# Kernel optimization log

Measured on AMD Instinct MI355X. Metric: run time of the kernel, lower is better.

## Reference

```python
import jax, jax.numpy as jnp
import numpy as np

N = 100000   # nodes
E = 1600000  # edges (avg degree 16)
IN, HID, OUT = 128, 128, 40


def setup_inputs() -> dict:
    key = jax.random.key(0)
    ks = jax.random.split(key, 7)
    return {
        "features": jax.random.normal(ks[0], (N, IN), jnp.float32),
        "src": jax.random.randint(ks[1], (E,), 0, N, jnp.int32),
        "dst": jax.random.randint(ks[2], (E,), 0, N, jnp.int32),
        "W1": jax.random.normal(ks[3], (IN, HID), jnp.float32) / np.sqrt(IN).astype(np.float32),
        "Wh": jax.random.normal(ks[4], (HID, HID), jnp.float32) / np.sqrt(HID).astype(np.float32),
        "W2": jax.random.normal(ks[5], (HID, OUT), jnp.float32) / np.sqrt(HID).astype(np.float32),
        "b2": jnp.zeros((OUT,), jnp.float32),
    }


def _agg(x, src, dst):
    # message passing: gather source node features along edges, sum-scatter to dst
    return jax.ops.segment_sum(x[src], dst, num_segments=N)


def reference(features, src, dst, W1, Wh, W2, b2):
    ones = jnp.ones((E,), jnp.float32)
    out_deg = jnp.clip(jax.ops.segment_sum(ones, src, num_segments=N), 1.0)
    in_deg = jnp.clip(jax.ops.segment_sum(ones, dst, num_segments=N), 1.0)
    lnorm = out_deg[:, None] ** -0.5  # 'both' left norm (src out-degree)
    rnorm = in_deg[:, None] ** -0.5   # 'both' right norm (dst in-degree)

    # conv1: GraphConv(norm='none', bias=False) -> plain sum aggregation, then relu
    h = jax.nn.relu(_agg(features @ W1, src, dst))
    # hidden GraphConv(norm='both', bias=False) + relu (dropout = identity in eval)
    h = jax.nn.relu(_agg((h * lnorm) @ Wh, src, dst) * rnorm)
    # conv2: GraphConv(norm='both', bias=True)
    h = _agg((h * lnorm) @ W2, src, dst) * rnorm + b2
    return jax.nn.log_softmax(h, axis=1)
```

## Files before the change

kernel.cpp:

```cpp
#include <hip/hip_runtime.h>
#include <math.h>

#define MAXDEG 64
#define BCAP 8192
#define EPB 4096

typedef __attribute__((ext_vector_type(8))) short bf16x8;
typedef __attribute__((ext_vector_type(4))) float f32x4;

static __device__ inline unsigned short f2bf(float f) {
    unsigned int u = __float_as_uint(f);
    u += 0x7FFFu + ((u >> 16) & 1u);
    return (unsigned short)(u >> 16);
}
static __device__ inline float bf2f(unsigned short u) {
    return __uint_as_float(((unsigned int)u) << 16);
}
static __device__ inline float4 ld_f4(const float* p) { return *(const float4*)p; }

static __device__ __forceinline__ void acc8(float* a, uint4 u) {
    a[0] += __uint_as_float(u.x << 16);
    a[1] += __uint_as_float(u.x & 0xFFFF0000u);
    a[2] += __uint_as_float(u.y << 16);
    a[3] += __uint_as_float(u.y & 0xFFFF0000u);
    a[4] += __uint_as_float(u.z << 16);
    a[5] += __uint_as_float(u.z & 0xFFFF0000u);
    a[6] += __uint_as_float(u.w << 16);
    a[7] += __uint_as_float(u.w & 0xFFFF0000u);
}

static __global__ __launch_bounds__(256) void wtrans_kernel(
    const float* __restrict__ W1, const float* __restrict__ Wh,
    const float* __restrict__ W2,
    unsigned short* __restrict__ W1t, unsigned short* __restrict__ WhT,
    unsigned short* __restrict__ Wt2) {
    int b = blockIdx.x;
    int t = threadIdx.x;
    if (b == 2) {
        for (int i = t; i < 48 * 128; i += 256) Wt2[i] = 0;
        __syncthreads();
        int n0 = (t & 31) * 4;
        if (n0 < 40) {
            for (int k = t >> 5; k < 128; k += 8) {
                float4 v = ld_f4(&W2[(size_t)k * 40 + n0]);
                Wt2[(size_t)(n0 + 0) * 128 + k] = f2bf(v.x);
                Wt2[(size_t)(n0 + 1) * 128 + k] = f2bf(v.y);
                Wt2[(size_t)(n0 + 2) * 128 + k] = f2bf(v.z);
                Wt2[(size_t)(n0 + 3) * 128 + k] = f2bf(v.w);
            }
        }
        return;
    }
    const float* Wsrc = (b == 0) ? W1 : Wh;
    unsigned short* Wdst = (b == 0) ? W1t : WhT;
    int n0 = (t & 31) * 4;
    for (int k = t >> 5; k < 128; k += 8) {
        float4 v = ld_f4(&Wsrc[(size_t)k * 128 + n0]);
        Wdst[(size_t)(n0 + 0) * 128 + k] = f2bf(v.x);
        Wdst[(size_t)(n0 + 1) * 128 + k] = f2bf(v.y);
        Wdst[(size_t)(n0 + 2) * 128 + k] = f2bf(v.z);
        Wdst[(size_t)(n0 + 3) * 128 + k] = f2bf(v.w);
    }
}

static __device__ __forceinline__ void gemm128_mfma256(
    const unsigned short* sa16, const unsigned short* __restrict__ Wt,
    unsigned short* __restrict__ Y, int row0, int t, int N) {
    int l = t & 63, w = t >> 6;
    int m = l & 15, kg = l >> 4;
    int row = w * 16 + m;
    int rsw = row & 15;
    f32x4 acc[8];
#pragma unroll
    for (int c = 0; c < 8; ++c) acc[c] = (f32x4){0.f, 0.f, 0.f, 0.f};
#pragma unroll
    for (int ks = 0; ks < 4; ++ks) {
        bf16x8 a = *(const bf16x8*)&sa16[(size_t)row * 128 + (((ks * 4 + kg) ^ rsw) * 8)];
        int kk = ks * 32 + kg * 8;
#pragma unroll
        for (int c = 0; c < 8; ++c) {
            bf16x8 b = *(const bf16x8*)&Wt[(size_t)(c * 16 + m) * 128 + kk];
            acc[c] = __builtin_amdgcn_mfma_f32_16x16x32_bf16(a, b, acc[c], 0, 0, 0);
        }
    }
#pragma unroll
    for (int c = 0; c < 8; ++c) {
        int col = c * 16 + m;
#pragma unroll
        for (int r = 0; r < 4; ++r) {
            int grow = row0 + w * 16 + kg * 4 + r;
            if (grow < N) Y[(size_t)grow * 128 + col] = f2bf(acc[c][r]);
        }
    }
}

static __device__ __forceinline__ void gemm128_mfma512(
    const unsigned short* sa16, const unsigned short* __restrict__ Wt,
    unsigned short* __restrict__ Y, int row0, int t, int N) {
    int l = t & 63, w = t >> 6;
    int rt = w >> 1, ctb = (w & 1) * 4;
    int m = l & 15, kg = l >> 4;
    int row = rt * 16 + m;
    int rsw = row & 15;
    f32x4 acc[4] = {{0.f, 0.f, 0.f, 0.f}, {0.f, 0.f, 0.f, 0.f},
                    {0.f, 0.f, 0.f, 0.f}, {0.f, 0.f, 0.f, 0.f}};
#pragma unroll
    for (int ks = 0; ks < 4; ++ks) {
        bf16x8 a = *(const bf16x8*)&sa16[(size_t)row * 128 + (((ks * 4 + kg) ^ rsw) * 8)];
        int kk = ks * 32 + kg * 8;
#pragma unroll
        for (int c = 0; c < 4; ++c) {
            int n = (ctb + c) * 16 + m;
            bf16x8 b = *(const bf16x8*)&Wt[(size_t)n * 128 + kk];
            acc[c] = __builtin_amdgcn_mfma_f32_16x16x32_bf16(a, b, acc[c], 0, 0, 0);
        }
    }
#pragma unroll
    for (int c = 0; c < 4; ++c) {
        int col = (ctb + c) * 16 + m;
#pragma unroll
        for (int r = 0; r < 4; ++r) {
            int grow = row0 + rt * 16 + kg * 4 + r;
            if (grow < N) Y[(size_t)grow * 128 + col] = f2bf(acc[c][r]);
        }
    }
}

static __device__ __forceinline__ void gemm40_mfma512(
    const unsigned short* sa16, const unsigned short* __restrict__ Wt2,
    unsigned short* __restrict__ Y3, int row0, int t, int N) {
    int l = t & 63, w = t >> 6;
    int rt = w & 3;
    int nct = (w < 4) ? 2 : 1;
    int ct0 = (w < 4) ? 0 : 2;
    int m = l & 15, kg = l >> 4;
    int row = rt * 16 + m;
    int rsw = row & 15;
    f32x4 acc[2] = {{0.f, 0.f, 0.f, 0.f}, {0.f, 0.f, 0.f, 0.f}};
#pragma unroll
    for (int ks = 0; ks < 4; ++ks) {
        bf16x8 a = *(const bf16x8*)&sa16[(size_t)row * 128 + (((ks * 4 + kg) ^ rsw) * 8)];
        int kk = ks * 32 + kg * 8;
        for (int c = 0; c < nct; ++c) {
            int n = (ct0 + c) * 16 + m;
            bf16x8 b = *(const bf16x8*)&Wt2[(size_t)n * 128 + kk];
            acc[c] = __builtin_amdgcn_mfma_f32_16x16x32_bf16(a, b, acc[c], 0, 0, 0);
        }
    }
    for (int c = 0; c < nct; ++c) {
        int col = (ct0 + c) * 16 + m;
        if (col >= 40) continue;
#pragma unroll
        for (int r = 0; r < 4; ++r) {
            int grow = row0 + rt * 16 + kg * 4 + r;
            if (grow < N) Y3[(size_t)grow * 40 + col] = f2bf(acc[c][r]);
        }
    }
}

template <int MODE>
static __device__ __forceinline__ void gather_phase(
    const unsigned short* __restrict__ Ysrc, unsigned short* sa16,
    const int* __restrict__ csr, const int* __restrict__ indeg,
    const int* __restrict__ outdeg, int row0, int t, int N) {
    int w = t >> 6;
    int l = t & 63;
    int q = l >> 4;
    int lq = l & 15;
    int qb = q * 16;

#pragma unroll
    for (int i = 0; i < 2; ++i) {
        int r = i * 32 + w * 4 + q;
        int node = row0 + r;
        bool valid = node < N;
        int d = 0;
        if (valid) d = indeg[node];
        int dc = d > MAXDEG ? MAXDEG : d;

        int idx0 = 0, idx1 = 0, idx2 = 0, idx3 = 0;
        if (valid) {
            const int* cp = csr + (size_t)node * MAXDEG;
            idx0 = cp[lq];
            if (dc > 16) idx1 = cp[16 + lq];
            if (dc > 32) idx2 = cp[32 + lq];
            if (dc > 48) idx3 = cp[48 + lq];
        }

        float a[8];
#pragma unroll
        for (int x = 0; x < 8; ++x) a[x] = 0.f;

#pragma unroll
        for (int c = 0; c < 4; ++c) {
            int ebase = c * 16;
            if (ebase >= dc) break;
            int v = (c == 0) ? idx0 : (c == 1) ? idx1 : (c == 2) ? idx2 : idx3;
            int lim = dc - ebase;
            if (lim > 16) lim = 16;
            int e = 0;
            for (; e + 4 <= lim; e += 4) {
                int s0 = __shfl(v, qb + e);
                int s1 = __shfl(v, qb + e + 1);
                int s2 = __shfl(v, qb + e + 2);
                int s3 = __shfl(v, qb + e + 3);
                uint4 u0 = *(const uint4*)&Ysrc[(size_t)s0 * 128 + lq * 8];
                uint4 u1 = *(const uint4*)&Ysrc[(size_t)s1 * 128 + lq * 8];
                uint4 u2 = *(const uint4*)&Ysrc[(size_t)s2 * 128 + lq * 8];
                uint4 u3 = *(const uint4*)&Ysrc[(size_t)s3 * 128 + lq * 8];
                acc8(a, u0); acc8(a, u1); acc8(a, u2); acc8(a, u3);
            }
            for (; e < lim; ++e) {
                int s0 = __shfl(v, qb + e);
                uint4 u0 = *(const uint4*)&Ysrc[(size_t)s0 * 128 + lq * 8];
                acc8(a, u0);
            }
        }

        if (valid) {
            int od = outdeg[node];
            float ln = rsqrtf((float)(od > 1 ? od : 1));
            if (MODE == 0) {
#pragma unroll
                for (int x = 0; x < 8; ++x) a[x] = fmaxf(a[x], 0.f) * ln;
            } else {
                float rn = rsqrtf((float)(d > 1 ? d : 1));
#pragma unroll
                for (int x = 0; x < 8; ++x) a[x] = fmaxf(a[x] * rn, 0.f) * ln;
            }
        }
        uint4 uo;
        uo.x = (unsigned)f2bf(a[0]) | ((unsigned)f2bf(a[1]) << 16);
        uo.y = (unsigned)f2bf(a[2]) | ((unsigned)f2bf(a[3]) << 16);
        uo.z = (unsigned)f2bf(a[4]) | ((unsigned)f2bf(a[5]) << 16);
        uo.w = (unsigned)f2bf(a[6]) | ((unsigned)f2bf(a[7]) << 16);
        int chunk = lq ^ (r & 15);
        *(uint4*)&sa16[(size_t)r * 128 + chunk * 8] = uo;
    }
}

static __global__ __launch_bounds__(256) void bucket_gemm1_kernel(
    const float* __restrict__ A, const unsigned short* __restrict__ W1t,
    unsigned short* __restrict__ Y,
    const int* __restrict__ src, const int* __restrict__ dst,
    int* __restrict__ cntD, int* __restrict__ cntS,
    unsigned int* __restrict__ bktD, unsigned char* __restrict__ bktS,
    int N, int E, int nb, int gG, int gB) {
    __shared__ unsigned short sa16[64 * 128];
    int bid = blockIdx.x;
    int t = threadIdx.x;

    int nI = 5 * gB;
    int role, idx;
    if (bid < nI) {
        if (bid % 5 == 0) { role = 1; idx = bid / 5; }
        else { role = 0; idx = bid - bid / 5 - 1; }
    } else { role = 0; idx = bid - gB; }
    if (role == 1 && idx >= gB) return;
    if (role == 0 && idx >= gG) return;

    if (role == 1) {
        int* sh = (int*)sa16;
        int* hD = sh;
        int* hS = sh + 512;
        int* bD = sh + 1024;
        int* bS = sh + 1536;
        int* cD = sh + 2048;
        int* cS = sh + 2560;
        for (int i = t; i < 512; i += 256) {
            hD[i] = 0; hS[i] = 0; cD[i] = 0; cS[i] = 0;
        }
        __syncthreads();

        int base = idx * EPB + t * 16;
        int s_r[16], d_r[16];
        int nv = 0;
        if (base + 16 <= E) {
            nv = 16;
#pragma unroll
            for (int k = 0; k < 4; ++k) {
                int4 sv = *(const int4*)&src[base + k * 4];
                int4 dv = *(const int4*)&dst[base + k * 4];
                s_r[k * 4 + 0] = sv.x; s_r[k * 4 + 1] = sv.y;
                s_r[k * 4 + 2] = sv.z; s_r[k * 4 + 3] = sv.w;
                d_r[k * 4 + 0] = dv.x; d_r[k * 4 + 1] = dv.y;
                d_r[k * 4 + 2] = dv.z; d_r[k * 4 + 3] = dv.w;
            }
        } else {
            nv = E - base; if (nv < 0) nv = 0; if (nv > 16) nv = 16;
#pragma unroll
            for (int k = 0; k < 16; ++k) {
                if (k < nv) { s_r[k] = src[base + k]; d_r[k] = dst[base + k]; }
                else { s_r[k] = 0; d_r[k] = 0; }
            }
        }

#pragma unroll
        for (int k = 0; k < 16; ++k) {
            if (k < nv) {
                atomicAdd(&hD[d_r[k] >> 8], 1);
                atomicAdd(&hS[s_r[k] >> 8], 1);
            }
        }
        __syncthreads();

        for (int b = t; b < nb; b += 256) {
            int h = hD[b];
            bD[b] = h ? atomicAdd(&cntD[b], h) : 0;
            int h2 = hS[b];
            bS[b] = h2 ? atomicAdd(&cntS[b], h2) : 0;
        }
        __syncthreads();

#pragma unroll
        for (int k = 0; k < 16; ++k) {
            if (k < nv) {
                int d = d_r[k], s = s_r[k];
                int bb = d >> 8;
                int p = atomicAdd(&cD[bb], 1) + bD[bb];
                if (p < BCAP)
                    bktD[(size_t)bb * BCAP + p] =
                        ((unsigned int)(d & 255) << 17) | (unsigned int)s;
                int sb = s >> 8;
                int p2 = atomicAdd(&cS[sb], 1) + bS[sb];
                if (p2 < BCAP)
                    bktS[(size_t)sb * BCAP + p2] = (unsigned char)(s & 255);
            }
        }
        return;
    }

    int row0 = idx * 64;
#pragma unroll
    for (int i = 0; i < 4; ++i) {
        int ci = i * 256 + t;
        int r = ci >> 4;
        int ch = ci & 15;
        int grow = row0 + r;
        uint4 uo = make_uint4(0u, 0u, 0u, 0u);
        if (grow < N) {
            float4 v0 = ld_f4(&A[(size_t)grow * 128 + ch * 8]);
            float4 v1 = ld_f4(&A[(size_t)grow * 128 + ch * 8 + 4]);
            uo.x = (unsigned)f2bf(v0.x) | ((unsigned)f2bf(v0.y) << 16);
            uo.y = (unsigned)f2bf(v0.z) | ((unsigned)f2bf(v0.w) << 16);
            uo.z = (unsigned)f2bf(v1.x) | ((unsigned)f2bf(v1.y) << 16);
            uo.w = (unsigned)f2bf(v1.z) | ((unsigned)f2bf(v1.w) << 16);
        }
        int chunk = ch ^ (r & 15);
        *(uint4*)&sa16[(size_t)r * 128 + chunk * 8] = uo;
    }
    __syncthreads();
    gemm128_mfma256(sa16, W1t, Y, row0, t, N);
}

static __global__ __launch_bounds__(256) void csr_build_kernel(
    const int* __restrict__ cntD, const int* __restrict__ cntS,
    const unsigned int* __restrict__ bktD, const unsigned char* __restrict__ bktS,
    int* __restrict__ csr, int* __restrict__ indeg, int* __restrict__ outdeg,
    int N, int nb) {
    __shared__ int cur[256];
    int bid = blockIdx.x;
    int t = threadIdx.x;
    cur[t] = 0;
    __syncthreads();

    if (bid < nb) {
        int b = bid;
        int cnt = cntD[b]; if (cnt > BCAP) cnt = BCAP;
        const unsigned int* bp = bktD + (size_t)b * BCAP;
        for (int i = t; i < cnt; i += 256) {
            unsigned int v = bp[i];
            int d8 = v >> 17;
            int s = (int)(v & 0x1FFFFu);
            int p = atomicAdd(&cur[d8], 1);
            if (p < MAXDEG) csr[((size_t)(b * 256 + d8)) * MAXDEG + p] = s;
        }
        __syncthreads();
        int node = b * 256 + t;
        if (node < N) indeg[node] = cur[t];
    } else {
        int b = bid - nb;
        int cnt = cntS[b]; if (cnt > BCAP) cnt = BCAP;
        const unsigned char* bp = bktS + (size_t)b * BCAP;
        for (int i = t; i < cnt; i += 256) atomicAdd(&cur[bp[i]], 1);
        __syncthreads();
        int node = b * 256 + t;
        if (node < N) outdeg[node] = cur[t];
    }
}

static __global__ __launch_bounds__(512) void agg_gemm2_kernel(
    const unsigned short* __restrict__ Y1, const unsigned short* __restrict__ WhT,
    unsigned short* __restrict__ Y2,
    const int* __restrict__ csr, const int* __restrict__ indeg,
    const int* __restrict__ outdeg, int N) {
    __shared__ unsigned short sa16[64 * 128];
    int t = threadIdx.x;
    int row0 = blockIdx.x * 64;
    gather_phase<0>(Y1, sa16, csr, indeg, outdeg, row0, t, N);
    __syncthreads();
    gemm128_mfma512(sa16, WhT, Y2, row0, t, N);
}

static __global__ __launch_bounds__(512) void agg_gemm3_kernel(
    const unsigned short* __restrict__ Y2, const unsigned short* __restrict__ Wt2,
    unsigned short* __restrict__ Y3,
    const int* __restrict__ csr, const int* __restrict__ indeg,
    const int* __restrict__ outdeg, int N) {
    __shared__ unsigned short sa16[64 * 128];
    int t = threadIdx.x;
    int row0 = blockIdx.x * 64;
    gather_phase<1>(Y2, sa16, csr, indeg, outdeg, row0, t, N);
    __syncthreads();
    gemm40_mfma512(sa16, Wt2, Y3, row0, t, N);
}

static __global__ __launch_bounds__(512) void agg40_lsm_kernel(
    const unsigned short* __restrict__ Y3, const float* __restrict__ b2,
    const int* __restrict__ csr, const int* __restrict__ indeg,
    float* __restrict__ out, int N) {
    int t = threadIdx.x;
    int node = blockIdx.x * 8 + (t >> 6);
    if (node >= N) return;
    int lane = t & 63;
    int grp = lane >> 4;
    int sub = lane & 15;
    int d = indeg[node];
    int dc = d > MAXDEG ? MAXDEG : d;

    float a0 = 0.f, a1 = 0.f, a2 = 0.f, a3 = 0.f;
    if (sub < 10) {
        const int* cp = csr + (size_t)node * MAXDEG;
        int e = grp;
        for (; e + 12 < dc; e += 16) {
            int s0 = cp[e];
            int s1 = cp[e + 4];
            int s2 = cp[e + 8];
            int s3 = cp[e + 12];
            ushort4 u0 = *(const ushort4*)&Y3[(size_t)s0 * 40 + sub * 4];
            ushort4 u1 = *(const ushort4*)&Y3[(size_t)s1 * 40 + sub * 4];
            ushort4 u2 = *(const ushort4*)&Y3[(size_t)s2 * 40 + sub * 4];
            ushort4 u3 = *(const ushort4*)&Y3[(size_t)s3 * 40 + sub * 4];
            a0 += bf2f(u0.x) + bf2f(u1.x) + bf2f(u2.x) + bf2f(u3.x);
            a1 += bf2f(u0.y) + bf2f(u1.y) + bf2f(u2.y) + bf2f(u3.y);
            a2 += bf2f(u0.z) + bf2f(u1.z) + bf2f(u2.z) + bf2f(u3.z);
            a3 += bf2f(u0.w) + bf2f(u1.w) + bf2f(u2.w) + bf2f(u3.w);
        }
        for (; e < dc; e += 4) {
            int s = cp[e];
            ushort4 u = *(const ushort4*)&Y3[(size_t)s * 40 + sub * 4];
            a0 += bf2f(u.x); a1 += bf2f(u.y); a2 += bf2f(u.z); a3 += bf2f(u.w);
        }
    }
    a0 += __shfl_xor(a0, 16); a0 += __shfl_xor(a0, 32);
    a1 += __shfl_xor(a1, 16); a1 += __shfl_xor(a1, 32);
    a2 += __shfl_xor(a2, 16); a2 += __shfl_xor(a2, 32);
    a3 += __shfl_xor(a3, 16); a3 += __shfl_xor(a3, 32);

    float rs = rsqrtf((float)(d > 1 ? d : 1));
    float x0 = 0.f, x1 = 0.f, x2 = 0.f, x3 = 0.f;
    float mx = -INFINITY;
    if (sub < 10) {
        float4 b = *(const float4*)&b2[sub * 4];
        x0 = a0 * rs + b.x;
        x1 = a1 * rs + b.y;
        x2 = a2 * rs + b.z;
        x3 = a3 * rs + b.w;
        mx = fmaxf(fmaxf(x0, x1), fmaxf(x2, x3));
    }
#pragma unroll
    for (int o = 1; o < 16; o <<= 1) mx = fmaxf(mx, __shfl_xor(mx, o));
    float ex = 0.f;
    if (sub < 10)
        ex = expf(x0 - mx) + expf(x1 - mx) + expf(x2 - mx) + expf(x3 - mx);
#pragma unroll
    for (int o = 1; o < 16; o <<= 1) ex += __shfl_xor(ex, o);
    float ls = logf(ex) + mx;
    if (sub < 10 && grp == 0)
        *(float4*)&out[(size_t)node * 40 + sub * 4] =
            make_float4(x0 - ls, x1 - ls, x2 - ls, x3 - ls);
}


extern "C" void kernel_launch(void* const* d_in, const int* in_sizes, int n_in,
                              void* d_out, int out_size, void* d_ws, size_t ws_size,
                              hipStream_t stream) {
    const float* features = (const float*)d_in[0];
    const int* src = (const int*)d_in[1];
    const int* dst = (const int*)d_in[2];
    const float* W1 = (const float*)d_in[3];
    const float* Wh = (const float*)d_in[4];
    const float* W2 = (const float*)d_in[5];
    const float* b2 = (const float*)d_in[6];
    float* out = (float*)d_out;

    const int N = in_sizes[0] / 128;
    const int E = in_sizes[1];
    const int nb = (N + 255) / 256;

    char* p = (char*)d_ws;
    auto carve = [&](size_t bytes) {
        char* q = p;
        p += (bytes + 255) & ~(size_t)255;
        return q;
    };
    unsigned short* bufY1 = (unsigned short*)carve((size_t)N * 128 * 2);
    unsigned short* bufY2 = (unsigned short*)carve((size_t)N * 128 * 2);
    unsigned short* bufY3 = (unsigned short*)carve((size_t)N * 40 * 2);
    int* csr = (int*)carve((size_t)N * MAXDEG * 4);
    unsigned int* bktD = (unsigned int*)carve((size_t)nb * BCAP * 4);
    unsigned char* bktS = (unsigned char*)carve((size_t)nb * BCAP);
    int* cntD = (int*)carve((size_t)nb * 4);
    int* cntS = (int*)carve((size_t)nb * 4);
    int* indeg = (int*)carve((size_t)N * 4);
    int* outdeg = (int*)carve((size_t)N * 4);
    unsigned short* W1t = (unsigned short*)carve((size_t)128 * 128 * 2);
    unsigned short* WhT = (unsigned short*)carve((size_t)128 * 128 * 2);
    unsigned short* Wt2 = (unsigned short*)carve((size_t)48 * 128 * 2);
    (void)ws_size; (void)n_in; (void)out_size;

    hipMemsetAsync(cntD, 0, (size_t)nb * 4, stream);
    hipMemsetAsync(cntS, 0, (size_t)nb * 4, stream);

    int gG = (N + 63) / 64;
    int gB = (E + EPB - 1) / EPB;
    wtrans_kernel<<<3, 256, 0, stream>>>(W1, Wh, W2, W1t, WhT, Wt2);
    bucket_gemm1_kernel<<<gG + gB, 256, 0, stream>>>(
        features, W1t, bufY1, src, dst, cntD, cntS, bktD, bktS, N, E, nb, gG, gB);
    csr_build_kernel<<<2 * nb, 256, 0, stream>>>(
        cntD, cntS, bktD, bktS, csr, indeg, outdeg, N, nb);
    agg_gemm2_kernel<<<gG, 512, 0, stream>>>(bufY1, WhT, bufY2, csr, indeg, outdeg, N);
    agg_gemm3_kernel<<<gG, 512, 0, stream>>>(bufY2, Wt2, bufY3, csr, indeg, outdeg, N);
    agg40_lsm_kernel<<<(N + 7) / 8, 512, 0, stream>>>(bufY3, b2, csr, indeg, out, N);
}
```

Measured before the change: 286.2 us.

## Quantize intermediate node features to int8 with per-row scales for gathers

The two 128-wide intermediate feature buffers written by the GEMM epilogues are now stored as int8 with a per-row float scale instead of bf16. The gather phases read 8 bytes per lane plus one scale per neighbor and dequantize while accumulating. This halves the bytes moved by the random-access neighbor gathers, which dominate the aggregation kernels. The cost is an extra row-max reduction (with shared atomics and a block sync in the 512-thread GEMM), an extra scale load per edge, and a loss of precision that may exceed tolerance.

Measured after the change: 270.3 us, median of 2. 1.06x faster.

```diff
diff --git a/kernel.cpp b/kernel.cpp
--- a/kernel.cpp
+++ b/kernel.cpp
@@ -18,15 +18,15 @@
 }
 static __device__ inline float4 ld_f4(const float* p) { return *(const float4*)p; }
 
-static __device__ __forceinline__ void acc8(float* a, uint4 u) {
-    a[0] += __uint_as_float(u.x << 16);
-    a[1] += __uint_as_float(u.x & 0xFFFF0000u);
-    a[2] += __uint_as_float(u.y << 16);
-    a[3] += __uint_as_float(u.y & 0xFFFF0000u);
-    a[4] += __uint_as_float(u.z << 16);
-    a[5] += __uint_as_float(u.z & 0xFFFF0000u);
-    a[6] += __uint_as_float(u.w << 16);
-    a[7] += __uint_as_float(u.w & 0xFFFF0000u);
+static __device__ __forceinline__ void acci8(float* a, uint2 u, float s) {
+    a[0] += s * (float)((int)(u.x << 24) >> 24);
+    a[1] += s * (float)((int)(u.x << 16) >> 24);
+    a[2] += s * (float)((int)(u.x << 8) >> 24);
+    a[3] += s * (float)((int)u.x >> 24);
+    a[4] += s * (float)((int)(u.y << 24) >> 24);
+    a[5] += s * (float)((int)(u.y << 16) >> 24);
+    a[6] += s * (float)((int)(u.y << 8) >> 24);
+    a[7] += s * (float)((int)u.y >> 24);
 }
 
 static __global__ __launch_bounds__(256) void wtrans_kernel(
@@ -63,9 +63,10 @@
     }
 }
 
-static __device__ __forceinline__ void gemm128_mfma256(
+static __device__ __forceinline__ void gemm128_mfma256_q(
     const unsigned short* sa16, const unsigned short* __restrict__ Wt,
-    unsigned short* __restrict__ Y, int row0, int t, int N) {
+    signed char* __restrict__ Y, float* __restrict__ sc,
+    int row0, int t, int N) {
     int l = t & 63, w = t >> 6;
     int m = l & 15, kg = l >> 4;
     int row = w * 16 + m;
@@ -84,19 +85,28 @@
         }
     }
 #pragma unroll
-    for (int c = 0; c < 8; ++c) {
-        int col = c * 16 + m;
-#pragma unroll
-        for (int r = 0; r < 4; ++r) {
-            int grow = row0 + w * 16 + kg * 4 + r;
-            if (grow < N) Y[(size_t)grow * 128 + col] = f2bf(acc[c][r]);
-        }
-    }
-}
-
-static __device__ __forceinline__ void gemm128_mfma512(
+    for (int r = 0; r < 4; ++r) {
+        float lm = 0.f;
+#pragma unroll
+        for (int c = 0; c < 8; ++c) lm = fmaxf(lm, fabsf(acc[c][r]));
+#pragma unroll
+        for (int o = 1; o < 16; o <<= 1) lm = fmaxf(lm, __shfl_xor(lm, o));
+        float inv = lm > 0.f ? 127.f / lm : 0.f;
+        int grow = row0 + w * 16 + kg * 4 + r;
+        if (grow < N) {
+#pragma unroll
+            for (int c = 0; c < 8; ++c)
+                Y[(size_t)grow * 128 + c * 16 + m] =
+                    (signed char)__float2int_rn(acc[c][r] * inv);
+            if (m == 0) sc[grow] = lm * (1.f / 127.f);
+        }
+    }
+}
+
+static __device__ __forceinline__ void gemm128_mfma512_q(
     const unsigned short* sa16, const unsigned short* __restrict__ Wt,
-    unsigned short* __restrict__ Y, int row0, int t, int N) {
+    signed char* __restrict__ Y, float* __restrict__ sc,
+    unsigned* rmaxu, int row0, int t, int N) {
     int l = t & 63, w = t >> 6;
     int rt = w >> 1, ctb = (w & 1) * 4;
     int m = l & 15, kg = l >> 4;
@@ -116,12 +126,28 @@
         }
     }
 #pragma unroll
-    for (int c = 0; c < 4; ++c) {
-        int col = (ctb + c) * 16 + m;
-#pragma unroll
-        for (int r = 0; r < 4; ++r) {
-            int grow = row0 + rt * 16 + kg * 4 + r;
-            if (grow < N) Y[(size_t)grow * 128 + col] = f2bf(acc[c][r]);
+    for (int r = 0; r < 4; ++r) {
+        float lm = 0.f;
+#pragma unroll
+        for (int c = 0; c < 4; ++c) lm = fmaxf(lm, fabsf(acc[c][r]));
+#pragma unroll
+        for (int o = 1; o < 16; o <<= 1) lm = fmaxf(lm, __shfl_xor(lm, o));
+        if (m == 0)
+            atomicMax(&rmaxu[rt * 16 + kg * 4 + r], __float_as_uint(lm));
+    }
+    __syncthreads();
+#pragma unroll
+    for (int r = 0; r < 4; ++r) {
+        int rl = rt * 16 + kg * 4 + r;
+        float am = __uint_as_float(rmaxu[rl]);
+        float inv = am > 0.f ? 127.f / am : 0.f;
+        int grow = row0 + rl;
+        if (grow < N) {
+#pragma unroll
+            for (int c = 0; c < 4; ++c)
+                Y[(size_t)grow * 128 + (ctb + c) * 16 + m] =
+                    (signed char)__float2int_rn(acc[c][r] * inv);
+            if (ctb == 0 && m == 0) sc[grow] = am * (1.f / 127.f);
         }
     }
 }
@@ -159,8 +185,9 @@
 }
 
 template <int MODE>
-static __device__ __forceinline__ void gather_phase(
-    const unsigned short* __restrict__ Ysrc, unsigned short* sa16,
+static __device__ __forceinline__ void gather_phase_i8(
+    const signed char* __restrict__ Ysrc, const float* __restrict__ scs,
+    unsigned short* sa16,
     const int* __restrict__ csr, const int* __restrict__ indeg,
     const int* __restrict__ outdeg, int row0, int t, int N) {
     int w = t >> 6;
@@ -204,16 +231,18 @@
                 int s1 = __shfl(v, qb + e + 1);
                 int s2 = __shfl(v, qb + e + 2);
                 int s3 = __shfl(v, qb + e + 3);
-                uint4 u0 = *(const uint4*)&Ysrc[(size_t)s0 * 128 + lq * 8];
-                uint4 u1 = *(const uint4*)&Ysrc[(size_t)s1 * 128 + lq * 8];
-                uint4 u2 = *(const uint4*)&Ysrc[(size_t)s2 * 128 + lq * 8];
-                uint4 u3 = *(const uint4*)&Ysrc[(size_t)s3 * 128 + lq * 8];
-                acc8(a, u0); acc8(a, u1); acc8(a, u2); acc8(a, u3);
+                uint2 u0 = *(const uint2*)&Ysrc[(size_t)s0 * 128 + lq * 8];
+                uint2 u1 = *(const uint2*)&Ysrc[(size_t)s1 * 128 + lq * 8];
+                uint2 u2 = *(const uint2*)&Ysrc[(size_t)s2 * 128 + lq * 8];
+                uint2 u3 = *(const uint2*)&Ysrc[(size_t)s3 * 128 + lq * 8];
+                float f0 = scs[s0], f1 = scs[s1], f2 = scs[s2], f3 = scs[s3];
+                acci8(a, u0, f0); acci8(a, u1, f1);
+                acci8(a, u2, f2); acci8(a, u3, f3);
             }
             for (; e < lim; ++e) {
                 int s0 = __shfl(v, qb + e);
-                uint4 u0 = *(const uint4*)&Ysrc[(size_t)s0 * 128 + lq * 8];
-                acc8(a, u0);
+                uint2 u0 = *(const uint2*)&Ysrc[(size_t)s0 * 128 + lq * 8];
+                acci8(a, u0, scs[s0]);
             }
         }
 
@@ -241,7 +270,7 @@
 
 static __global__ __launch_bounds__(256) void bucket_gemm1_kernel(
     const float* __restrict__ A, const unsigned short* __restrict__ W1t,
-    unsigned short* __restrict__ Y,
+    signed char* __restrict__ Y, float* __restrict__ s1,
     const int* __restrict__ src, const int* __restrict__ dst,
     int* __restrict__ cntD, int* __restrict__ cntS,
     unsigned int* __restrict__ bktD, unsigned char* __restrict__ bktS,
@@ -350,7 +379,7 @@
         *(uint4*)&sa16[(size_t)r * 128 + chunk * 8] = uo;
     }
     __syncthreads();
-    gemm128_mfma256(sa16, W1t, Y, row0, t, N);
+    gemm128_mfma256_q(sa16, W1t, Y, s1, row0, t, N);
 }
 
 static __global__ __launch_bounds__(256) void csr_build_kernel(
@@ -390,27 +419,31 @@
 }
 
 static __global__ __launch_bounds__(512) void agg_gemm2_kernel(
-    const unsigned short* __restrict__ Y1, const unsigned short* __restrict__ WhT,
-    unsigned short* __restrict__ Y2,
+    const signed char* __restrict__ Y1, const float* __restrict__ s1,
+    const unsigned short* __restrict__ WhT,
+    signed char* __restrict__ Y2, float* __restrict__ s2,
     const int* __restrict__ csr, const int* __restrict__ indeg,
     const int* __restrict__ outdeg, int N) {
     __shared__ unsigned short sa16[64 * 128];
+    __shared__ unsigned rmaxu[64];
     int t = threadIdx.x;
+    if (t < 64) rmaxu[t] = 0u;
     int row0 = blockIdx.x * 64;
-    gather_phase<0>(Y1, sa16, csr, indeg, outdeg, row0, t, N);
+    gather_phase_i8<0>(Y1, s1, sa16, csr, indeg, outdeg, row0, t, N);
     __syncthreads();
-    gemm128_mfma512(sa16, WhT, Y2, row0, t, N);
+    gemm128_mfma512_q(sa16, WhT, Y2, s2, rmaxu, row0, t, N);
 }
 
 static __global__ __launch_bounds__(512) void agg_gemm3_kernel(
-    const unsigned short* __restrict__ Y2, const unsigned short* __restrict__ Wt2,
+    const signed char* __restrict__ Y2, const float* __restrict__ s2,
+    const unsigned short* __restrict__ Wt2,
     unsigned short* __restrict__ Y3,
     const int* __restrict__ csr, const int* __restrict__ indeg,
     const int* __restrict__ outdeg, int N) {
     __shared__ unsigned short sa16[64 * 128];
     int t = threadIdx.x;
     int row0 = blockIdx.x * 64;
-    gather_phase<1>(Y2, sa16, csr, indeg, outdeg, row0, t, N);
+    gather_phase_i8<1>(Y2, s2, sa16, csr, indeg, outdeg, row0, t, N);
     __syncthreads();
     gemm40_mfma512(sa16, Wt2, Y3, row0, t, N);
 }
@@ -504,8 +537,10 @@
         p += (bytes + 255) & ~(size_t)255;
         return q;
     };
-    unsigned short* bufY1 = (unsigned short*)carve((size_t)N * 128 * 2);
-    unsigned short* bufY2 = (unsigned short*)carve((size_t)N * 128 * 2);
+    signed char* bufY1 = (signed char*)carve((size_t)N * 128);
+    float* sc1 = (float*)carve((size_t)N * 4);
+    signed char* bufY2 = (signed char*)carve((size_t)N * 128);
+    float* sc2 = (float*)carve((size_t)N * 4);
     unsigned short* bufY3 = (unsigned short*)carve((size_t)N * 40 * 2);
     int* csr = (int*)carve((size_t)N * MAXDEG * 4);
     unsigned int* bktD = (unsigned int*)carve((size_t)nb * BCAP * 4);
@@ -526,10 +561,13 @@
     int gB = (E + EPB - 1) / EPB;
     wtrans_kernel<<<3, 256, 0, stream>>>(W1, Wh, W2, W1t, WhT, Wt2);
     bucket_gemm1_kernel<<<gG + gB, 256, 0, stream>>>(
-        features, W1t, bufY1, src, dst, cntD, cntS, bktD, bktS, N, E, nb, gG, gB);
+        features, W1t, bufY1, sc1, src, dst, cntD, cntS, bktD, bktS,
+        N, E, nb, gG, gB);
     csr_build_kernel<<<2 * nb, 256, 0, stream>>>(
         cntD, cntS, bktD, bktS, csr, indeg, outdeg, N, nb);
-    agg_gemm2_kernel<<<gG, 512, 0, stream>>>(bufY1, WhT, bufY2, csr, indeg, outdeg, N);
-    agg_gemm3_kernel<<<gG, 512, 0, stream>>>(bufY2, Wt2, bufY3, csr, indeg, outdeg, N);
+    agg_gemm2_kernel<<<gG, 512, 0, stream>>>(bufY1, sc1, WhT, bufY2, sc2,
+                                             csr, indeg, outdeg, N);
+    agg_gemm3_kernel<<<gG, 512, 0, stream>>>(bufY2, sc2, Wt2, bufY3,
+                                             csr, indeg, outdeg, N);
     agg40_lsm_kernel<<<(N + 7) / 8, 512, 0, stream>>>(bufY3, b2, csr, indeg, out, N);
 }
```
